# Performance work log

Measured on AMD Instinct MI355X. Metric: run time of the kernel, lower is better.

The kernel has to match this reference:

```python
import jax, jax.numpy as jnp
import numpy as np

B, H, W, C = 2, 128, 128, 256
WS = 8            # current_window (query window)
KW = 16           # halo_window = 2*current_window
HEADS = 8
HD = C // HEADS
PRETRAIN = 8
CPB_HIDDEN = 512


def _rel_bias_consts():
    halo = (KW - WS) // 2
    coords = np.arange(1 - WS - halo, WS + halo, dtype=np.float32)  # length WS+KW-1 = 23
    tab = np.stack(np.meshgrid(coords, coords, indexing='ij'), axis=-1)  # [23,23,2]
    tab = tab * (8.0 / (PRETRAIN - 1.0))
    tab = np.sign(tab) * np.log1p(np.abs(tab)) / np.log(8.0)
    tab = tab.reshape(-1, 2).astype(np.float32)                      # [529,2]
    qi = np.arange(WS)
    qg = np.stack(np.meshgrid(qi, qi, indexing='ij')).reshape(2, -1)  # [2,64]
    ki = np.arange(KW)
    kg = np.stack(np.meshgrid(ki, ki, indexing='ij')).reshape(2, -1)  # [2,256]
    rel = qg[:, :, None] - kg[:, None] + (KW - 1)
    idx = (rel[0] * (WS + KW - 1) + rel[1]).reshape(-1).astype(np.int32)  # [64*256]
    return tab, idx

_REL_TAB, _REL_IDX = _rel_bias_consts()


def setup_inputs() -> dict:
    key = jax.random.key(0)
    ks = jax.random.split(key, 12)
    s = 0.02
    return {
        'x': jax.random.normal(ks[0], (B, H, W, C), jnp.float32),
        'w_qkv': jax.random.normal(ks[1], (C, 3 * C), jnp.float32) * s,
        'w_dw': jax.random.normal(ks[2], (3, 3, 1, 3 * C), jnp.float32) * s,  # depthwise HWIO
        'ln_g': jnp.ones((3 * C,), jnp.float32),
        'ln_b': jnp.zeros((3 * C,), jnp.float32),
        'q_bias': jnp.zeros((C,), jnp.float32),
        'v_bias': jnp.zeros((C,), jnp.float32),
        'logit_scale': jnp.full((HEADS, 1, 1), np.log(10.0), jnp.float32),
        'cpb_w1': jax.random.normal(ks[3], (2, CPB_HIDDEN), jnp.float32) * s,
        'cpb_b1': jnp.zeros((CPB_HIDDEN,), jnp.float32),
        'cpb_w2': jax.random.normal(ks[4], (CPB_HIDDEN, HEADS), jnp.float32) * s,
        'w_proj': jax.random.normal(ks[5], (C, C), jnp.float32) * s,
    }


def _l2n(t):
    # tf.math.l2_normalize with epsilon=1.55e-5
    return t * jax.lax.rsqrt(jnp.maximum(jnp.sum(t * t, -1, keepdims=True), 1.55e-5))


def reference(x, w_qkv, w_dw, ln_g, ln_b, q_bias, v_bias, logit_scale,
              cpb_w1, cpb_b1, cpb_w2, w_proj):
    nWh, nWw = H // WS, W // WS
    nW = nWh * nWw
    # qkv 1x1 conv + depthwise 3x3 + layernorm + (q,0,v) bias
    qkv = jnp.einsum('bhwc,cd->bhwd', x, w_qkv)
    qkv = jax.lax.conv_general_dilated(
        qkv, w_dw, (1, 1), 'SAME',
        dimension_numbers=('NHWC', 'HWIO', 'NHWC'), feature_group_count=3 * C)
    mu = jnp.mean(qkv, -1, keepdims=True)
    var = jnp.var(qkv, -1, keepdims=True)
    qkv = (qkv - mu) * jax.lax.rsqrt(var + 1e-5) * ln_g + ln_b
    qkv = qkv + jnp.concatenate([q_bias, jnp.zeros_like(q_bias), v_bias])
    q, kv = qkv[..., :C], qkv[..., C:]
    # window partition of q: [B*nW, heads, WS*WS, HD]
    qp = q.reshape(B, nWh, WS, nWw, WS, HEADS, HD)
    qp = qp.transpose(0, 1, 3, 5, 2, 4, 6).reshape(B * nW, HEADS, WS * WS, HD)
    # halo partition of kv: overlapping KWxKW patches, stride WS
    halo = (KW - WS) // 2
    kvp = jnp.pad(kv, ((0, 0), (halo, halo), (halo, halo), (0, 0)))
    ridx = (np.arange(nWh) * WS)[:, None] + np.arange(KW)[None]  # [nWh,KW]
    cidx = (np.arange(nWw) * WS)[:, None] + np.arange(KW)[None]  # [nWw,KW]
    kvp = kvp[:, ridx][:, :, :, cidx]               # [B,nWh,KW,nWw,KW,2C]
    kvp = kvp.transpose(0, 1, 3, 2, 4, 5).reshape(B * nW, KW * KW, 2, HEADS, HD)
    k = kvp[:, :, 0].transpose(0, 2, 1, 3)          # [B*nW, heads, KW*KW, HD]
    v = kvp[:, :, 1].transpose(0, 2, 1, 3)
    # cosine attention with clamped learned log-scale
    scale = jnp.exp(jnp.minimum(logit_scale, np.float32(np.log(100.0))))
    attn = jnp.einsum('whqd,whkd->whqk', _l2n(qp) * scale, _l2n(k))
    # continuous relative position bias (CPB MLP + gather)
    hidden = jax.nn.relu(jnp.asarray(_REL_TAB) @ cpb_w1 + cpb_b1)
    bias_tab = jax.nn.sigmoid(hidden @ cpb_w2) * 16.0        # [529, heads]
    rb = bias_tab[_REL_IDX].reshape(WS * WS, KW * KW, HEADS).transpose(2, 0, 1)
    attn = jax.nn.softmax(attn + rb[None], axis=-1)
    out = jnp.einsum('whqk,whkd->whqd', attn, v)             # [B*nW, heads, 64, HD]
    # reverse window partition
    out = out.reshape(B, nWh, nWw, HEADS, WS, WS, HD)
    out = out.transpose(0, 1, 4, 2, 5, 3, 6).reshape(B, H, W, C)
    return jnp.einsum('bhwc,cd->bhwd', out, w_proj)
```

## Files before the change

### kernel.cpp

```cpp
#include <hip/hip_runtime.h>
#include <hip/hip_bf16.h>
#include <hip/hip_fp16.h>
#include <cstddef>
#include <cstdint>

#define BB 2
#define HH 128
#define WW 128
#define CC 256
#define WSZ 8
#define KWIN 16
#define NHEADS 8
#define HD 32
#define C3 768
#define NPIX 32768
#define NWIN 512

typedef short    bf16x8 __attribute__((ext_vector_type(8)));
typedef _Float16 half8  __attribute__((ext_vector_type(8)));
typedef float    f32x4  __attribute__((ext_vector_type(4)));

__device__ inline short f2bf(float f) {
    union { float f; unsigned u; } v; v.f = f;
    unsigned r = (v.u + 0x7fffu + ((v.u >> 16) & 1u)) >> 16;
    return (short)r;
}

__device__ inline void gload_lds16(const _Float16* g, _Float16* l) {
    __builtin_amdgcn_global_load_lds(
        (const __attribute__((address_space(1))) unsigned int*)g,
        (__attribute__((address_space(3))) unsigned int*)l, 16, 0, 0);
}

__global__ __launch_bounds__(64) void cpb_kernel(const float* __restrict__ w1,
                                                 const float* __restrict__ b1,
                                                 const float* __restrict__ w2,
                                                 float* __restrict__ btab) {
    const int e = blockIdx.x;
    const int i = e / 23, j = e % 23;
    const float inv_log8 = 1.0f / logf(8.0f);
    float c0 = (float)(i - 11) * (8.0f / 7.0f);
    float c1 = (float)(j - 11) * (8.0f / 7.0f);
    float f0 = copysignf(log1pf(fabsf(c0)) * inv_log8, c0);
    float f1 = copysignf(log1pf(fabsf(c1)) * inv_log8, c1);

    const int t = threadIdx.x;
    float acc[8] = {0.f,0.f,0.f,0.f,0.f,0.f,0.f,0.f};
    for (int kk = 0; kk < 8; kk++) {
        int k = kk * 64 + t;
        float hid = f0 * w1[k] + f1 * w1[512 + k] + b1[k];
        hid = fmaxf(hid, 0.f);
        #pragma unroll
        for (int h = 0; h < 8; h++) acc[h] += hid * w2[k * 8 + h];
    }
    #pragma unroll
    for (int h = 0; h < 8; h++) {
        #pragma unroll
        for (int off = 32; off >= 1; off >>= 1) acc[h] += __shfl_xor(acc[h], off);
    }
    if (t < 8) {
        float v = acc[t];
        btab[e * 8 + t] = 16.0f / (1.0f + expf(-v));
    }
}

__global__ __launch_bounds__(256) void cvt_wdw(const float* __restrict__ src,
                                               _Float16* __restrict__ dst) {
    int i = blockIdx.x * 256 + threadIdx.x;
    if (i < 9 * C3) dst[i] = (_Float16)src[i];
}

__global__ __launch_bounds__(256) void transpose_cvt(const float* __restrict__ src,
                                                     _Float16* __restrict__ dst,
                                                     int R, int Cn) {
    __shared__ float t[32][33];
    const int bx = blockIdx.x, by = blockIdx.y;
    const int tx = threadIdx.x & 31, ty = threadIdx.x >> 5;
    #pragma unroll
    for (int i = 0; i < 4; i++) {
        int r = by * 32 + ty + i * 8;
        t[ty + i * 8][tx] = src[(size_t)r * Cn + bx * 32 + tx];
    }
    __syncthreads();
    #pragma unroll
    for (int i = 0; i < 4; i++) {
        int dr = bx * 32 + ty + i * 8;
        dst[(size_t)dr * R + by * 32 + tx] = (_Float16)t[tx][ty + i * 8];
    }
}

template <typename OT>
__global__ __launch_bounds__(256) void gemm_f16(const _Float16* __restrict__ A,
                                                const _Float16* __restrict__ Bt,
                                                OT* __restrict__ C,
                                                int M, int N, int K) {
    __shared__ _Float16 Ash[128][64];
    __shared__ _Float16 Bsh[128][64];
    const int tid = threadIdx.x;
    const int wv = tid >> 6, ln = tid & 63;
    const int quad = ln >> 4, l15 = ln & 15;
    const int rowb = blockIdx.y * 128;
    const int colb = blockIdx.x * 128;
    const int wm = (wv >> 1) * 64, wn = (wv & 1) * 64;

    const int r8 = ln >> 3, g = ln & 7;
    const int kg = g ^ r8;

    f32x4 acc[4][4] = {};
    for (int k0 = 0; k0 < K; k0 += 64) {
        #pragma unroll
        for (int i = 0; i < 4; i++) {
            const int m = wv * 32 + i * 8 + r8;
            gload_lds16(A + (size_t)(rowb + m) * K + k0 + kg * 8,
                        &Ash[wv * 32 + i * 8][0]);
            gload_lds16(Bt + (size_t)(colb + m) * K + k0 + kg * 8,
                        &Bsh[wv * 32 + i * 8][0]);
        }
        __syncthreads();
        #pragma unroll
        for (int kk = 0; kk < 2; kk++) {
            const int phys = ((kk * 4 + quad) ^ (l15 & 7)) * 8;
            half8 a[4], b[4];
            #pragma unroll
            for (int i = 0; i < 4; i++)
                a[i] = *(const half8*)&Ash[wm + i * 16 + l15][phys];
            #pragma unroll
            for (int j = 0; j < 4; j++)
                b[j] = *(const half8*)&Bsh[wn + j * 16 + l15][phys];
            #pragma unroll
            for (int i = 0; i < 4; i++)
                #pragma unroll
                for (int j = 0; j < 4; j++)
                    acc[i][j] = __builtin_amdgcn_mfma_f32_16x16x32_f16(
                        a[i], b[j], acc[i][j], 0, 0, 0);
        }
        __syncthreads();
    }
    #pragma unroll
    for (int i = 0; i < 4; i++) {
        #pragma unroll
        for (int reg = 0; reg < 4; reg++) {
            const size_t row = rowb + wm + i * 16 + quad * 4 + reg;
            #pragma unroll
            for (int j = 0; j < 4; j++) {
                C[row * N + colb + wn + j * 16 + l15] = (OT)acc[i][j][reg];
            }
        }
    }
}

__global__ __launch_bounds__(256) void gemm_qkv(const float* __restrict__ A,
                                                const _Float16* __restrict__ Bt,
                                                _Float16* __restrict__ C,
                                                int M, int N, int K) {
    __shared__ _Float16 Ash[128][64];
    __shared__ _Float16 Bsh[128][64];
    const int tid = threadIdx.x;
    const int wv = tid >> 6, ln = tid & 63;
    const int quad = ln >> 4, l15 = ln & 15;
    const int rowb = blockIdx.y * 128;
    const int colb = blockIdx.x * 128;
    const int wm = (wv >> 1) * 64, wn = (wv & 1) * 64;
    const int r8 = ln >> 3, g = ln & 7;
    const int kg = g ^ r8;

    f32x4 acc[4][4] = {};
    for (int k0 = 0; k0 < K; k0 += 64) {
        #pragma unroll
        for (int i = 0; i < 4; i++) {
            const int m = wv * 32 + i * 8 + r8;
            const float* ap = A + (size_t)(rowb + m) * K + k0 + g * 8;
            const float4 a0 = *(const float4*)ap;
            const float4 a1 = *(const float4*)(ap + 4);
            half8 hv;
            hv[0] = (_Float16)a0.x; hv[1] = (_Float16)a0.y;
            hv[2] = (_Float16)a0.z; hv[3] = (_Float16)a0.w;
            hv[4] = (_Float16)a1.x; hv[5] = (_Float16)a1.y;
            hv[6] = (_Float16)a1.z; hv[7] = (_Float16)a1.w;
            *(half8*)&Ash[wv * 32 + i * 8 + r8][kg * 8] = hv;
            gload_lds16(Bt + (size_t)(colb + m) * K + k0 + kg * 8,
                        &Bsh[wv * 32 + i * 8][0]);
        }
        __syncthreads();
        #pragma unroll
        for (int kk = 0; kk < 2; kk++) {
            const int phys = ((kk * 4 + quad) ^ (l15 & 7)) * 8;
            half8 a[4], b[4];
            #pragma unroll
            for (int i = 0; i < 4; i++)
                a[i] = *(const half8*)&Ash[wm + i * 16 + l15][phys];
            #pragma unroll
            for (int j = 0; j < 4; j++)
                b[j] = *(const half8*)&Bsh[wn + j * 16 + l15][phys];
            #pragma unroll
            for (int i = 0; i < 4; i++)
                #pragma unroll
                for (int j = 0; j < 4; j++)
                    acc[i][j] = __builtin_amdgcn_mfma_f32_16x16x32_f16(
                        a[i], b[j], acc[i][j], 0, 0, 0);
        }
        __syncthreads();
    }
    #pragma unroll
    for (int i = 0; i < 4; i++) {
        #pragma unroll
        for (int reg = 0; reg < 4; reg++) {
            const size_t row = rowb + wm + i * 16 + quad * 4 + reg;
            #pragma unroll
            for (int j = 0; j < 4; j++) {
                C[row * N + colb + wn + j * 16 + l15] = (_Float16)acc[i][j][reg];
            }
        }
    }
}

__global__ __launch_bounds__(256) void dwconv_ln(const _Float16* __restrict__ in,
                                                 const _Float16* __restrict__ wdwh,
                                                 const float* __restrict__ g,
                                                 const float* __restrict__ bt,
                                                 const float* __restrict__ qb,
                                                 const float* __restrict__ vb,
                                                 _Float16* __restrict__ out) {
    __shared__ _Float16 S[2880 * 8];
    __shared__ float sred[4][8][2];

    const int t = threadIdx.x;
    const int pix0 = blockIdx.x * 8;
    const int b = pix0 >> 14, y = (pix0 >> 7) & 127, x0 = pix0 & 127;

    for (int u = t; u < 2880; u += 256) {
        const int r = u / 960, rem = u - r * 960;
        const int c = rem / 96, grp = rem - c * 96;
        const int yy = y + r - 1, xx = x0 + c - 1;
        half8 v = (half8)(_Float16)0;
        if ((unsigned)yy < 128u && (unsigned)xx < 128u)
            v = *(const half8*)(in + (((size_t)(b * 128 + yy) * 128 + xx) * C3)
                                + grp * 8);
        const int phys = (u & ~7) | ((u ^ c) & 7);
        *(half8*)&S[phys * 8] = v;
    }
    __syncthreads();

    const int p = t & 7, gidx = t >> 3;
    float acc[3][8] = {};
    #pragma unroll
    for (int s = 0; s < 3; s++) {
        const int grp = gidx + s * 32;
        half8 w[9];
        #pragma unroll
        for (int tap = 0; tap < 9; tap++)
            w[tap] = *(const half8*)(wdwh + (tap * 96 + grp) * 8);
        #pragma unroll
        for (int r = 0; r < 3; r++) {
            #pragma unroll
            for (int dx = 0; dx < 3; dx++) {
                const int c = p + dx;
                const int u = (r * 10 + c) * 96 + grp;
                const int phys = (u & ~7) | ((u ^ c) & 7);
                const half8 v = *(const half8*)&S[phys * 8];
                const half8 wt = w[r * 3 + dx];
                #pragma unroll
                for (int i = 0; i < 8; i++)
                    acc[s][i] += (float)v[i] * (float)wt[i];
            }
        }
    }

    float ls = 0.f, lss = 0.f;
    #pragma unroll
    for (int s = 0; s < 3; s++)
        #pragma unroll
        for (int i = 0; i < 8; i++) { ls += acc[s][i]; lss += acc[s][i] * acc[s][i]; }
    ls  += __shfl_xor(ls, 8);  lss += __shfl_xor(lss, 8);
    ls  += __shfl_xor(ls, 16); lss += __shfl_xor(lss, 16);
    ls  += __shfl_xor(ls, 32); lss += __shfl_xor(lss, 32);
    const int wv = t >> 6, lnid = t & 63;
    if (lnid < 8) { sred[wv][lnid][0] = ls; sred[wv][lnid][1] = lss; }
    __syncthreads();
    const float Ssum  = sred[0][p][0] + sred[1][p][0] + sred[2][p][0] + sred[3][p][0];
    const float SSsum = sred[0][p][1] + sred[1][p][1] + sred[2][p][1] + sred[3][p][1];
    const float mu  = Ssum * (1.0f / 768.0f);
    const float var = SSsum * (1.0f / 768.0f) - mu * mu;
    const float rs  = rsqrtf(var + 1e-5f);

    const size_t obase = (size_t)(pix0 + p) * C3;
    #pragma unroll
    for (int s = 0; s < 3; s++) {
        const int ch = gidx * 8 + s * 256;
        const float4 g0 = *(const float4*)(g + ch);
        const float4 g1 = *(const float4*)(g + ch + 4);
        const float4 b0 = *(const float4*)(bt + ch);
        const float4 b1 = *(const float4*)(bt + ch + 4);
        float gg[8] = {g0.x, g0.y, g0.z, g0.w, g1.x, g1.y, g1.z, g1.w};
        float bb[8] = {b0.x, b0.y, b0.z, b0.w, b1.x, b1.y, b1.z, b1.w};
        if (s == 0) {
            const float4 e0 = *(const float4*)(qb + ch);
            const float4 e1 = *(const float4*)(qb + ch + 4);
            bb[0] += e0.x; bb[1] += e0.y; bb[2] += e0.z; bb[3] += e0.w;
            bb[4] += e1.x; bb[5] += e1.y; bb[6] += e1.z; bb[7] += e1.w;
        } else if (s == 2) {
            const float4 e0 = *(const float4*)(vb + ch - 512);
            const float4 e1 = *(const float4*)(vb + ch - 512 + 4);
            bb[0] += e0.x; bb[1] += e0.y; bb[2] += e0.z; bb[3] += e0.w;
            bb[4] += e1.x; bb[5] += e1.y; bb[6] += e1.z; bb[7] += e1.w;
        }
        if (s == 2) {
            bf16x8 o;
            #pragma unroll
            for (int i = 0; i < 8; i++)
                o[i] = f2bf((acc[s][i] - mu) * rs * gg[i] + bb[i]);
            *(bf16x8*)((short*)(out + obase + ch)) = o;
        } else {
            half8 o;
            #pragma unroll
            for (int i = 0; i < 8; i++)
                o[i] = (_Float16)((acc[s][i] - mu) * rs * gg[i] + bb[i]);
            *(half8*)(out + obase + ch) = o;
        }
    }
}

__global__ __launch_bounds__(256) void attn_mfma(const _Float16* __restrict__ qkv,
                                                 const float* __restrict__ bias_tab,
                                                 const float* __restrict__ logit_scale,
                                                 _Float16* __restrict__ out) {
    const int blk = blockIdx.x;
    const int h = blk & 7;
    const int wid = blk >> 3;
    const int b = wid >> 8;
    const int wy = (wid >> 4) & 15;
    const int wx = wid & 15;
    const int tid = threadIdx.x;
    const int wave = tid >> 6, lane = tid & 63;
    const int quad = lane >> 4, l15 = lane & 15;

    __shared__ _Float16 Bf[16 * 64 * 8];
    __shared__ short Vt[32][264];
    __shared__ short Pl[4][16][128];
    __shared__ float btab[529];

    const float lscale = __expf(fminf(logit_scale[h], 4.60517019f));
    const float Mshift = lscale + 16.0f;
    for (int e = tid; e < 529; e += 256) btab[e] = bias_tab[e * 8 + h] - Mshift;

    {
        const int j = tid;
        const int kr = j >> 4, kcc = j & 15;
        const int gy = wy * 8 - 4 + kr, gx = wx * 8 - 4 + kcc;
        const bool inb = ((unsigned)gy < 128u) && ((unsigned)gx < 128u);
        const _Float16* p = qkv +
            (((size_t)(b * 128 + (inb ? gy : 0)) * 128 + (inb ? gx : 0)) * C3) +
            256 + h * HD;
        const short* vp = (const short*)(p + 256);
        float kreg[32];
        float s2 = 0.f;
        #pragma unroll
        for (int d8 = 0; d8 < 4; d8++) {
            half8 kk;
            bf16x8 vv;
            if (inb) { kk = *(const half8*)(p + d8 * 8); vv = *(const bf16x8*)(vp + d8 * 8); }
            else     { kk = (half8)(_Float16)0;          vv = (bf16x8)(short)0; }
            #pragma unroll
            for (int u = 0; u < 8; u++) {
                const float kf = (float)kk[u];
                kreg[d8 * 8 + u] = kf;
                s2 += kf * kf;
                Vt[d8 * 8 + u][j] = vv[u];
            }
        }
        const float r = rsqrtf(fmaxf(s2, 1.55e-5f));
        #pragma unroll
        for (int d8 = 0; d8 < 4; d8++) {
            half8 hv;
            #pragma unroll
            for (int u = 0; u < 8; u++)
                hv[u] = (_Float16)(kreg[d8 * 8 + u] * r);
            *(half8*)&Bf[(((j >> 4) * 64) + d8 * 16 + (j & 15)) * 8] = hv;
        }
    }
    __syncthreads();

    const int qrow = wave * 16 + l15;
    const int qr = qrow >> 3, qc = qrow & 7;
    const int qy = wy * 8 + qr, qx = wx * 8 + qc;
    half8 afrag;
    {
        const _Float16* qp = qkv + (((size_t)(b * 128 + qy) * 128 + qx) * C3) + h * HD + quad * 8;
        half8 q8 = *(const half8*)qp;
        float qf[8];
        float s2 = 0.f;
        #pragma unroll
        for (int u = 0; u < 8; u++) { qf[u] = (float)q8[u]; s2 += qf[u] * qf[u]; }
        s2 += __shfl_xor(s2, 16);
        s2 += __shfl_xor(s2, 32);
        const float rq = rsqrtf(fmaxf(s2, 1.55e-5f)) * lscale;
        #pragma unroll
        for (int u = 0; u < 8; u++) afrag[u] = (_Float16)(qf[u] * rq);
    }

    float lsum[4] = {0.f, 0.f, 0.f, 0.f};
    f32x4 d0 = {0.f, 0.f, 0.f, 0.f};
    f32x4 d1 = {0.f, 0.f, 0.f, 0.f};
    #pragma unroll
    for (int hf = 0; hf < 2; hf++) {
        #pragma unroll
        for (int ntl = 0; ntl < 8; ntl++) {
            const int nt = hf * 8 + ntl;
            half8 bfrag = *(const half8*)&Bf[(nt * 64 + lane) * 8];
            f32x4 s = {0.f, 0.f, 0.f, 0.f};
            s = __builtin_amdgcn_mfma_f32_16x16x32_f16(afrag, bfrag, s, 0, 0, 0);
            #pragma unroll
            for (int reg = 0; reg < 4; reg++) {
                const int q  = quad * 4 + reg;
                const int gq = wave * 16 + q;
                const int rqr = gq >> 3, rqc = gq & 7;
                const float rb = btab[(rqr - nt + 15) * 23 + (rqc - l15 + 15)];
                const float pv = __expf(s[reg] + rb);
                lsum[reg] += pv;
                Pl[wave][q][(ntl * 16 + l15) ^ ((q & 12) << 2)] = f2bf(pv);
            }
        }
        #pragma unroll
        for (int ch = 0; ch < 4; ch++) {
            const int kb = hf * 128 + ch * 32;
            bf16x8 pa = *(const bf16x8*)&Pl[wave][l15][(ch * 32 + quad * 8) ^ ((l15 & 12) << 2)];
            bf16x8 b0 = *(const bf16x8*)&Vt[l15][kb + quad * 8];
            bf16x8 b1 = *(const bf16x8*)&Vt[l15 + 16][kb + quad * 8];
            d0 = __builtin_amdgcn_mfma_f32_16x16x32_bf16(pa, b0, d0, 0, 0, 0);
            d1 = __builtin_amdgcn_mfma_f32_16x16x32_bf16(pa, b1, d1, 0, 0, 0);
        }
    }
    #pragma unroll
    for (int reg = 0; reg < 4; reg++) {
        float v = lsum[reg];
        v += __shfl_xor(v, 1); v += __shfl_xor(v, 2);
        v += __shfl_xor(v, 4); v += __shfl_xor(v, 8);
        lsum[reg] = 1.0f / v;
    }

    #pragma unroll
    for (int reg = 0; reg < 4; reg++) {
        const int gq = wave * 16 + quad * 4 + reg;
        const int oqr = gq >> 3, oqc = gq & 7;
        const int oy = wy * 8 + oqr, ox = wx * 8 + oqc;
        _Float16* op = out + (((size_t)(b * 128 + oy) * 128 + ox) * CC) + h * HD;
        op[l15]      = (_Float16)(d0[reg] * lsum[reg]);
        op[16 + l15] = (_Float16)(d1[reg] * lsum[reg]);
    }
}

extern "C" void kernel_launch(void* const* d_in, const int* in_sizes, int n_in,
                              void* d_out, int out_size, void* d_ws, size_t ws_size,
                              hipStream_t stream) {
    const float* x           = (const float*)d_in[0];
    const float* w_qkv       = (const float*)d_in[1];
    const float* w_dw        = (const float*)d_in[2];
    const float* ln_g        = (const float*)d_in[3];
    const float* ln_b        = (const float*)d_in[4];
    const float* q_bias      = (const float*)d_in[5];
    const float* v_bias      = (const float*)d_in[6];
    const float* logit_scale = (const float*)d_in[7];
    const float* cpb_w1      = (const float*)d_in[8];
    const float* cpb_b1      = (const float*)d_in[9];
    const float* cpb_w2      = (const float*)d_in[10];
    const float* w_proj      = (const float*)d_in[11];
    float* out = (float*)d_out;

    char* ws = (char*)d_ws;
    _Float16* qkv0h  = (_Float16*)(ws);
    _Float16* qkvh   = (_Float16*)(ws + 50331648);
    _Float16* attnh  = (_Float16*)(ws + 100663296);
    _Float16* wqkvT  = (_Float16*)(ws + 117440512);
    _Float16* wprojT = (_Float16*)(ws + 117833728);
    _Float16* wdwh   = (_Float16*)(ws + 117964800);
    float*    btab   = (float*)   (ws + 117981184);

    cpb_kernel<<<529, 64, 0, stream>>>(cpb_w1, cpb_b1, cpb_w2, btab);
    cvt_wdw<<<27, 256, 0, stream>>>(w_dw, wdwh);
    transpose_cvt<<<dim3(C3 / 32, CC / 32), 256, 0, stream>>>(w_qkv, wqkvT, CC, C3);
    transpose_cvt<<<dim3(CC / 32, CC / 32), 256, 0, stream>>>(w_proj, wprojT, CC, CC);

    gemm_qkv<<<dim3(C3 / 128, NPIX / 128), 256, 0, stream>>>(
        x, wqkvT, qkv0h, NPIX, C3, CC);
    dwconv_ln<<<NPIX / 8, 256, 0, stream>>>(qkv0h, wdwh, ln_g, ln_b, q_bias,
                                            v_bias, qkvh);
    attn_mfma<<<NWIN * NHEADS, 256, 0, stream>>>(qkvh, btab, logit_scale, attnh);
    gemm_f16<float><<<dim3(CC / 128, NPIX / 128), 256, 0, stream>>>(
        attnh, wprojT, out, NPIX, CC, CC);
}
```

Before: 253.1 us.

## Precompute bias in MFMA fragment layout and fold into accumulator with exp2

Adds a small kernel that lays out the relative position bias per head directly in MFMA output-fragment order, pre-shifted and scaled by log2(e). The attention kernel feeds this bias as the initial MFMA accumulator and uses exp2f, with the query scale also multiplied by log2(e). This removes the per-block LDS bias table fill and the per-element index math and gather. It also replaces round-to-nearest bf16 conversion of probabilities with truncation and drops the XOR swizzle in favour of padding the P buffer. The cost is an extra global f32x4 load per tile (L2-resident, 512 KB total) and slightly less accurate probabilities from truncation.

```diff
diff --git a/kernel.cpp b/kernel.cpp
--- a/kernel.cpp
+++ b/kernel.cpp
@@ -62,6 +62,22 @@
         float v = acc[t];
         btab[e * 8 + t] = 16.0f / (1.0f + expf(-v));
     }
+}
+
+__global__ __launch_bounds__(64) void rbfrag_kernel(const float* __restrict__ btab,
+                                                    const float* __restrict__ logit_scale,
+                                                    float* __restrict__ rbf) {
+    const int blk = blockIdx.x;
+    const int h = blk >> 6, nt = (blk >> 2) & 15, w = blk & 3;
+    const int lane = threadIdx.x, quad = lane >> 4, l15 = lane & 15;
+    const float M = __expf(fminf(logit_scale[h], 4.60517019f)) + 16.0f;
+    const int row = w * 2 + (quad >> 1) + 15 - nt;
+    const int colb = (quad & 1) * 4 + 15 - l15;
+    f32x4 v;
+    #pragma unroll
+    for (int reg = 0; reg < 4; reg++)
+        v[reg] = (btab[(row * 23 + colb + reg) * 8 + h] - M) * 1.44269504f;
+    *(f32x4*)(rbf + (size_t)blk * 256 + lane * 4) = v;
 }
 
 __global__ __launch_bounds__(256) void cvt_wdw(const float* __restrict__ src,
@@ -321,7 +337,7 @@
 }
 
 __global__ __launch_bounds__(256) void attn_mfma(const _Float16* __restrict__ qkv,
-                                                 const float* __restrict__ bias_tab,
+                                                 const float* __restrict__ rbf,
                                                  const float* __restrict__ logit_scale,
                                                  _Float16* __restrict__ out) {
     const int blk = blockIdx.x;
@@ -336,12 +352,9 @@
 
     __shared__ _Float16 Bf[16 * 64 * 8];
     __shared__ short Vt[32][264];
-    __shared__ short Pl[4][16][128];
-    __shared__ float btab[529];
+    __shared__ short Pl[4][16][136];
 
     const float lscale = __expf(fminf(logit_scale[h], 4.60517019f));
-    const float Mshift = lscale + 16.0f;
-    for (int e = tid; e < 529; e += 256) btab[e] = bias_tab[e * 8 + h] - Mshift;
 
     {
         const int j = tid;
@@ -393,10 +406,12 @@
         for (int u = 0; u < 8; u++) { qf[u] = (float)q8[u]; s2 += qf[u] * qf[u]; }
         s2 += __shfl_xor(s2, 16);
         s2 += __shfl_xor(s2, 32);
-        const float rq = rsqrtf(fmaxf(s2, 1.55e-5f)) * lscale;
+        const float rq = rsqrtf(fmaxf(s2, 1.55e-5f)) * lscale * 1.44269504f;
         #pragma unroll
         for (int u = 0; u < 8; u++) afrag[u] = (_Float16)(qf[u] * rq);
     }
+
+    const float* rbp = rbf + ((size_t)(h * 16) * 4 + wave) * 256 + lane * 4;
 
     float lsum[4] = {0.f, 0.f, 0.f, 0.f};
     f32x4 d0 = {0.f, 0.f, 0.f, 0.f};
@@ -406,24 +421,21 @@
         #pragma unroll
         for (int ntl = 0; ntl < 8; ntl++) {
             const int nt = hf * 8 + ntl;
+            const f32x4 c = *(const f32x4*)(rbp + nt * 1024);
             half8 bfrag = *(const half8*)&Bf[(nt * 64 + lane) * 8];
-            f32x4 s = {0.f, 0.f, 0.f, 0.f};
-            s = __builtin_amdgcn_mfma_f32_16x16x32_f16(afrag, bfrag, s, 0, 0, 0);
+            f32x4 s = __builtin_amdgcn_mfma_f32_16x16x32_f16(afrag, bfrag, c, 0, 0, 0);
             #pragma unroll
             for (int reg = 0; reg < 4; reg++) {
-                const int q  = quad * 4 + reg;
-                const int gq = wave * 16 + q;
-                const int rqr = gq >> 3, rqc = gq & 7;
-                const float rb = btab[(rqr - nt + 15) * 23 + (rqc - l15 + 15)];
-                const float pv = __expf(s[reg] + rb);
+                const float pv = exp2f(s[reg]);
                 lsum[reg] += pv;
-                Pl[wave][q][(ntl * 16 + l15) ^ ((q & 12) << 2)] = f2bf(pv);
+                union { float f; unsigned u; } pb; pb.f = pv;
+                Pl[wave][quad * 4 + reg][ntl * 16 + l15] = (short)(pb.u >> 16);
             }
         }
         #pragma unroll
         for (int ch = 0; ch < 4; ch++) {
             const int kb = hf * 128 + ch * 32;
-            bf16x8 pa = *(const bf16x8*)&Pl[wave][l15][(ch * 32 + quad * 8) ^ ((l15 & 12) << 2)];
+            bf16x8 pa = *(const bf16x8*)&Pl[wave][l15][ch * 32 + quad * 8];
             bf16x8 b0 = *(const bf16x8*)&Vt[l15][kb + quad * 8];
             bf16x8 b1 = *(const bf16x8*)&Vt[l15 + 16][kb + quad * 8];
             d0 = __builtin_amdgcn_mfma_f32_16x16x32_bf16(pa, b0, d0, 0, 0, 0);
@@ -474,8 +486,10 @@
     _Float16* wprojT = (_Float16*)(ws + 117833728);
     _Float16* wdwh   = (_Float16*)(ws + 117964800);
     float*    btab   = (float*)   (ws + 117981184);
+    float*    rbf    = (float*)   (ws + 118013952);
 
     cpb_kernel<<<529, 64, 0, stream>>>(cpb_w1, cpb_b1, cpb_w2, btab);
+    rbfrag_kernel<<<512, 64, 0, stream>>>(btab, logit_scale, rbf);
     cvt_wdw<<<27, 256, 0, stream>>>(w_dw, wdwh);
     transpose_cvt<<<dim3(C3 / 32, CC / 32), 256, 0, stream>>>(w_qkv, wqkvT, CC, C3);
     transpose_cvt<<<dim3(CC / 32, CC / 32), 256, 0, stream>>>(w_proj, wprojT, CC, CC);
@@ -484,7 +498,7 @@
         x, wqkvT, qkv0h, NPIX, C3, CC);
     dwconv_ln<<<NPIX / 8, 256, 0, stream>>>(qkv0h, wdwh, ln_g, ln_b, q_bias,
                                             v_bias, qkvh);
-    attn_mfma<<<NWIN * NHEADS, 256, 0, stream>>>(qkvh, btab, logit_scale, attnh);
+    attn_mfma<<<NWIN * NHEADS, 256, 0, stream>>>(qkvh, rbf, logit_scale, attnh);
     gemm_f16<float><<<dim3(CC / 128, NPIX / 128), 256, 0, stream>>>(
         attnh, wprojT, out, NPIX, CC, CC);
 }
```

Result: no change. 257.2 us (+1.6%).
